# Performance work log

Hardware: AMD Instinct MI355X
Metric: run time of the kernel (lower is better)

Reference implementation:

```python
import jax, jax.numpy as jnp
import numpy as np

B, D, E, C = 16384, 768, 124, 6  # batch, emb_dim, n_experts, n_classes


def _mlp(h, w1, b1, w2, b2):
    # timm Mlp: fc1 -> GELU(exact) -> fc2, hidden = in_features
    return jax.nn.gelu(h @ w1 + b1, approximate=False) @ w2 + b2


def setup_inputs() -> dict:
    key = jax.random.key(0)
    ks = jax.random.split(key, 14)
    s = 0.02
    inp = {
        "x": jax.random.normal(ks[0], (B, D), dtype=jnp.float32),
        # per-sample expert counts in [1, E]
        "n_experts": jax.random.randint(ks[1], (B,), 1, E + 1, dtype=jnp.int64 if jax.config.jax_enable_x64 else jnp.int32),
        # classifier Mlp: D -> D -> E*C
        "cls_w1": jax.random.normal(ks[2], (D, D), dtype=jnp.float32) * s,
        "cls_b1": jnp.zeros((D,), jnp.float32),
        "cls_w2": jax.random.normal(ks[3], (D, E * C), dtype=jnp.float32) * s,
        "cls_b2": jnp.zeros((E * C,), jnp.float32),
        # which_expert Mlp: D -> D -> E
        "we_w1": jax.random.normal(ks[4], (D, D), dtype=jnp.float32) * s,
        "we_b1": jnp.zeros((D,), jnp.float32),
        "we_w2": jax.random.normal(ks[5], (D, E), dtype=jnp.float32) * s,
        "we_b2": jnp.zeros((E,), jnp.float32),
        # expert_weights Mlp: D -> D -> E
        "ew_w1": jax.random.normal(ks[6], (D, D), dtype=jnp.float32) * s,
        "ew_b1": jnp.zeros((D,), jnp.float32),
        "ew_w2": jax.random.normal(ks[7], (D, E), dtype=jnp.float32) * s,
        "ew_b2": jnp.zeros((E,), jnp.float32),
    }
    return inp


def reference(x, n_experts, cls_w1, cls_b1, cls_w2, cls_b2,
              we_w1, we_b1, we_w2, we_b2, ew_w1, ew_b1, ew_w2, ew_b2):
    emb = x  # backbone = identity
    expert_logits = _mlp(emb, cls_w1, cls_b1, cls_w2, cls_b2).reshape(B, E, C)
    expert_weight_logits = _mlp(emb, ew_w1, ew_b1, ew_w2, ew_b2)  # [B, E]
    which_expert = _mlp(emb, we_w1, we_b1, we_w2, we_b2)          # [B, E]

    n = jnp.minimum(n_experts, E)                                  # clamp to n_experts
    # kth_largest: sort descending, pick (n-1)-th per row -> threshold
    sorted_desc = -jnp.sort(-which_expert, axis=1)
    threshold = sorted_desc[jnp.arange(B), n - 1][:, None]         # [B, 1]
    mask = which_expert < threshold

    expert_weight_logits = jnp.where(mask, -jnp.inf, expert_weight_logits)
    expert_proba = jax.nn.softmax(expert_logits, axis=2)           # over classes
    expert_weights = jax.nn.softmax(expert_weight_logits, axis=1)  # over experts

    combined = (expert_proba * expert_weights[:, :, None]).sum(axis=1)
    return combined / expert_weights.sum(axis=1)[:, None]          # [B, C]
```

## Files before the change

kernel.cpp:

```cpp
#include <hip/hip_runtime.h>
#include <stdint.h>

typedef unsigned short u16;
typedef short short8 __attribute__((ext_vector_type(8)));
typedef float f32x4 __attribute__((ext_vector_type(4)));

#define NB 16384

#define OFF_XHI      0ull
#define OFF_XLO      25165824ull
#define OFF_LCLS     0ull
#define OFF_LWE_P0   25165824ull
#define OFF_LWE_P1   33554432ull
#define OFF_BT1      50331648ull
#define OFF_LEWB     50331648ull
#define OFF_BTWE_HI  52690944ull
#define OFF_BTWE_LO  53870592ull
#define OFF_BT2CLS   55050240ull
#define OFF_BT2EW    56229888ull
#define OFF_BT2WE_HI 56426496ull
#define OFF_BT2WE_LO 56623104ull
#define OFF_B1CE     56819712ull
#define OFF_B1WE     56825856ull
#define OFF_B2CLS    56828928ull
#define OFF_B2EW     56832000ull
#define OFF_B2WE     56832512ull
#define OFF_HCLSEW   56833024ull
#define OFF_HWE_HI   107164672ull
#define OFF_HWE_LO   132330496ull
#define WS_NEED      157496320ull

__device__ __forceinline__ u16 f2bf(float f) {
  uint32_t u = __float_as_uint(f);
  u += 0x7fffu + ((u >> 16) & 1u);
  return (u16)(u >> 16);
}
__device__ __forceinline__ float bf2f(u16 h) {
  return __uint_as_float(((uint32_t)h) << 16);
}
__device__ __forceinline__ uint32_t pk2(float a, float b) {
  return (uint32_t)f2bf(a) | ((uint32_t)f2bf(b) << 16);
}
__device__ __forceinline__ void g2l16(const u16* g, u16* l) {
  __builtin_amdgcn_global_load_lds(
      (__attribute__((address_space(1))) void*)(u16*)g,
      (__attribute__((address_space(3))) void*)l, 16, 0, 0);
}

__device__ __forceinline__ float gelu_exact(float v) {
  const float x = fabsf(v) * 0.70710678118654752f;
  const float t = __fdividef(1.0f, __builtin_fmaf(0.3275911f, x, 1.0f));
  float p = __builtin_fmaf(1.061405429f, t, -1.453152027f);
  p = __builtin_fmaf(p, t, 1.421413741f);
  p = __builtin_fmaf(p, t, -0.284496736f);
  p = __builtin_fmaf(p, t, 0.254829592f);
  p = p * t;
  const float e = __expf(-x * x);
  float erfx = __builtin_fmaf(-p, e, 1.0f);
  erfx = (v < 0.f) ? -erfx : erfx;
  return 0.5f * v * (1.0f + erfx);
}

__global__ void prep_all(
    const float* __restrict__ x, u16* __restrict__ xhi, u16* __restrict__ xlo,
    const float* __restrict__ cls_w1, const float* __restrict__ ew_w1,
    const float* __restrict__ we_w1,  const float* __restrict__ cls_w2,
    const float* __restrict__ ew_w2,  const float* __restrict__ we_w2,
    u16* BT1, u16* BTwe_hi, u16* BTwe_lo,
    u16* BT2cls, u16* BT2ew, u16* BT2we_hi, u16* BT2we_lo,
    const float* __restrict__ cls_b1, const float* __restrict__ ew_b1,
    const float* __restrict__ we_b1,  const float* __restrict__ cls_b2,
    const float* __restrict__ ew_b2,  const float* __restrict__ we_b2,
    float* b1ce, float* b1we, float* b2cls, float* b2ew, float* b2we) {
  __shared__ float t[64][65];
  const int bid = blockIdx.x;
  if (bid < 12288) {
    int i = bid * 256 + threadIdx.x;
    float4 v = ((const float4*)x)[i];
    ushort4 h, l;
    h.x = f2bf(v.x); l.x = f2bf(v.x - bf2f(h.x));
    h.y = f2bf(v.y); l.y = f2bf(v.y - bf2f(h.y));
    h.z = f2bf(v.z); l.z = f2bf(v.z - bf2f(h.z));
    h.w = f2bf(v.w); l.w = f2bf(v.w - bf2f(h.w));
    ((ushort4*)xhi)[i] = h;
    ((ushort4*)xlo)[i] = l;
    return;
  }
  if (bid < 13152) {
    const int idx = bid - 12288;
    const int bx = idx % 12, by = (idx / 12) % 12, bz = idx / 144;
    const float* src; int N; u16* dhi; u16* dlo = nullptr;
    switch (bz) {
      case 0: src = cls_w1; N = 768; dhi = BT1; break;
      case 1: src = ew_w1;  N = 768; dhi = BT1 + 768 * 768; break;
      case 2: src = we_w1;  N = 768; dhi = BTwe_hi; dlo = BTwe_lo; break;
      case 3: src = cls_w2; N = 744; dhi = BT2cls; break;
      case 4: src = ew_w2;  N = 124; dhi = BT2ew; break;
      default: src = we_w2; N = 124; dhi = BT2we_hi; dlo = BT2we_lo; break;
    }
    const int Npad = (N + 127) & ~127;
    const int n0 = by * 64;
    if (n0 >= Npad) return;
    const int k0 = bx * 64;
    const int tx = threadIdx.x & 63, tg = threadIdx.x >> 6;
#pragma unroll
    for (int r = 0; r < 16; ++r) {
      int k = tg * 16 + r;
      int n = n0 + tx;
      t[k][tx] = (n < N) ? src[(size_t)(k0 + k) * N + n] : 0.f;
    }
    __syncthreads();
#pragma unroll
    for (int r = 0; r < 16; ++r) {
      int n = n0 + tg * 16 + r;
      if (n < Npad) {
        float v = t[tx][tg * 16 + r];
        u16 h = f2bf(v);
        dhi[(size_t)n * 768 + k0 + tx] = h;
        if (dlo) dlo[(size_t)n * 768 + k0 + tx] = f2bf(v - bf2f(h));
      }
    }
    return;
  }
  int id = (bid - 13152) * 256 + threadIdx.x;
  if (id < 1536) { b1ce[id] = (id < 768) ? cls_b1[id] : ew_b1[id - 768]; return; }
  id -= 1536;
  if (id < 768) { b1we[id] = we_b1[id]; return; }
  id -= 768;
  if (id < 768) { b2cls[id] = (id < 744) ? cls_b2[id] : 0.f; return; }
  id -= 768;
  if (id < 128) { b2ew[id] = (id < 124) ? ew_b2[id] : 0.f; return; }
  id -= 128;
  if (id < 128) { b2we[id] = (id < 124) ? we_b2[id] : 0.f; return; }
}

__device__ __forceinline__ void gemm_core(
    const u16* A0, const u16* A1, const u16* A2, int lda,
    const u16* B0, const u16* B1, const u16* B2,
    int npass, int K, int bm, int tid, u16* sA, u16* sB, f32x4 acc[4][4]) {
  const int lane = tid & 63;
  const int wv = tid >> 6;
  const int wr = wv >> 1, wc = wv & 1;
  const int sr = lane >> 3;
  const int sc = (((lane & 7) ^ sr) << 3);
  for (int p = 0; p < npass; ++p) {
    const u16* A = (p == 0) ? A0 : ((p == 1) ? A1 : A2);
    const u16* Bp = (p == 0) ? B0 : ((p == 1) ? B1 : B2);
    const u16* gA = A + (size_t)(bm + wv * 32 + sr) * lda + sc;
    const u16* gB = Bp + (size_t)(wv * 32 + sr) * K + sc;
    u16* lA = sA + (wv * 32) * 64;
    u16* lB = sB + (wv * 32) * 64;
    for (int kt = 0; kt < K; kt += 64) {
#pragma unroll
      for (int s = 0; s < 4; ++s) {
        g2l16(gA + (size_t)(s * 8) * lda + kt, lA + s * 8 * 64);
        g2l16(gB + (size_t)(s * 8) * K + kt, lB + s * 8 * 64);
      }
      __syncthreads();
#pragma unroll
      for (int ks = 0; ks < 2; ++ks) {
        const int co = ((ks * 4 + (lane >> 4)) ^ (lane & 7)) * 8;
        short8 av[4], bv[4];
#pragma unroll
        for (int i = 0; i < 4; i++)
          av[i] = *(const short8*)(sA + (wr * 64 + i * 16 + (lane & 15)) * 64 + co);
#pragma unroll
        for (int j = 0; j < 4; j++)
          bv[j] = *(const short8*)(sB + (wc * 64 + j * 16 + (lane & 15)) * 64 + co);
#pragma unroll
        for (int i = 0; i < 4; i++)
#pragma unroll
          for (int j = 0; j < 4; j++)
            acc[i][j] = __builtin_amdgcn_mfma_f32_16x16x32_bf16(bv[j], av[i], acc[i][j], 0, 0, 0);
      }
      __syncthreads();
    }
  }
}

__device__ __forceinline__ void gemm_split_core(
    const u16* __restrict__ Ahi, const u16* __restrict__ Alo, int lda,
    const u16* __restrict__ Bhi, const u16* __restrict__ Blo, int ldb,
    int K, int bm, int tid, u16* sA, u16* sB, f32x4 acc[4][4]) {
  const int lane = tid & 63;
  const int wv = tid >> 6;
  const int wr = wv >> 1, wc = wv & 1;
  const int sr = lane >> 3;
  const int gl = (lane & 7) ^ sr;
  const int koff = (gl & 3) << 3;
  const u16* Asel = (gl < 4) ? Ahi : Alo;
  const u16* Bsel = (gl < 4) ? Bhi : Blo;
  const u16* gA = Asel + (size_t)(bm + wv * 32 + sr) * lda + koff;
  const u16* gB = Bsel + (size_t)(wv * 32 + sr) * ldb + koff;
  u16* lA = sA + (wv * 32) * 64;
  u16* lB = sB + (wv * 32) * 64;

  for (int kt = 0; kt < K; kt += 32) {
#pragma unroll
    for (int s = 0; s < 4; ++s) {
      g2l16(gA + (size_t)(s * 8) * lda + kt, lA + s * 8 * 64);
      g2l16(gB + (size_t)(s * 8) * ldb + kt, lB + s * 8 * 64);
    }
    __syncthreads();
    const int coh = (((lane >> 4) ^ (lane & 7)) << 3);
    short8 ah[4], al[4], bh[4], bl[4];
#pragma unroll
    for (int i = 0; i < 4; i++) {
      const u16* p = sA + (wr * 64 + i * 16 + (lane & 15)) * 64;
      ah[i] = *(const short8*)(p + coh);
      al[i] = *(const short8*)(p + (coh ^ 32));
    }
#pragma unroll
    for (int j = 0; j < 4; j++) {
      const u16* p = sB + (wc * 64 + j * 16 + (lane & 15)) * 64;
      bh[j] = *(const short8*)(p + coh);
      bl[j] = *(const short8*)(p + (coh ^ 32));
    }
#pragma unroll
    for (int i = 0; i < 4; i++)
#pragma unroll
      for (int j = 0; j < 4; j++) {
        acc[i][j] = __builtin_amdgcn_mfma_f32_16x16x32_bf16(bh[j], ah[i], acc[i][j], 0, 0, 0);
        acc[i][j] = __builtin_amdgcn_mfma_f32_16x16x32_bf16(bh[j], al[i], acc[i][j], 0, 0, 0);
        acc[i][j] = __builtin_amdgcn_mfma_f32_16x16x32_bf16(bl[j], ah[i], acc[i][j], 0, 0, 0);
      }
    __syncthreads();
  }
}

__device__ __forceinline__ void decode_bid(int bid, int NC, int& bm, int& bn) {
  const int xcd = bid & 7, slot = bid >> 3;
  const int per = NC << 3;
  const int sub = slot / per, rem = slot - sub * per;
  const int colu = rem >> 3, rowIn = rem & 7;
  bm = ((xcd << 4) + (sub << 3) + rowIn) << 7;
  bn = colu << 7;
}

__global__ __launch_bounds__(256, 4) void gemm1_fused(
    const u16* __restrict__ Ahi, const u16* __restrict__ Alo,
    const u16* __restrict__ Bwe_hi, const u16* __restrict__ Bwe_lo,
    const u16* __restrict__ BT1,
    const float* __restrict__ b1we, const float* __restrict__ b1ce,
    u16* __restrict__ out_we_hi, u16* __restrict__ out_we_lo,
    u16* __restrict__ out_ce) {
  __shared__ u16 smem[2 * 128 * 64];
  u16* sA = smem;
  u16* sB = smem + 128 * 64;
  const int tid = threadIdx.x;
  const int lane = tid & 63;
  const int wr = (tid >> 6) >> 1, wc = (tid >> 6) & 1;
  const int K = 768;

  f32x4 acc[4][4];
#pragma unroll
  for (int i = 0; i < 4; i++)
#pragma unroll
    for (int j = 0; j < 4; j++) acc[i][j] = f32x4{0.f, 0.f, 0.f, 0.f};

  if (blockIdx.x < 768) {
    int bm, bn;
    decode_bid(blockIdx.x, 6, bm, bn);
    gemm_split_core(Ahi, Alo, K, Bwe_hi + (size_t)bn * K, Bwe_lo + (size_t)bn * K, K,
                    K, bm, tid, sA, sB, acc);
#pragma unroll
    for (int i = 0; i < 4; i++) {
      const int row = bm + wr * 64 + i * 16 + (lane & 15);
      u16* rh = out_we_hi + (size_t)row * 768;
      u16* rl = out_we_lo + (size_t)row * 768;
#pragma unroll
      for (int j = 0; j < 4; j++) {
        const int colb = bn + wc * 64 + j * 16 + ((lane >> 4) << 2);
        const float4 bs = *(const float4*)(b1we + colb);
        float g0 = gelu_exact(acc[i][j][0] + bs.x);
        float g1 = gelu_exact(acc[i][j][1] + bs.y);
        float g2 = gelu_exact(acc[i][j][2] + bs.z);
        float g3 = gelu_exact(acc[i][j][3] + bs.w);
        uint2 hv, lv;
        u16 h0 = f2bf(g0), h1 = f2bf(g1), h2 = f2bf(g2), h3 = f2bf(g3);
        hv.x = (uint32_t)h0 | ((uint32_t)h1 << 16);
        hv.y = (uint32_t)h2 | ((uint32_t)h3 << 16);
        lv.x = pk2(g0 - bf2f(h0), g1 - bf2f(h1));
        lv.y = pk2(g2 - bf2f(h2), g3 - bf2f(h3));
        *(uint2*)(rh + colb) = hv;
        *(uint2*)(rl + colb) = lv;
      }
    }
  } else {
    int bm, bn;
    decode_bid(blockIdx.x - 768, 12, bm, bn);
    gemm_core(Ahi, nullptr, nullptr, 768, BT1 + (size_t)bn * K, nullptr, nullptr,
              1, K, bm, tid, sA, sB, acc);
#pragma unroll
    for (int i = 0; i < 4; i++) {
      const int row = bm + wr * 64 + i * 16 + (lane & 15);
      u16* ro = out_ce + (size_t)row * 1536;
#pragma unroll
      for (int j = 0; j < 4; j++) {
        const int colb = bn + wc * 64 + j * 16 + ((lane >> 4) << 2);
        const float4 bs = *(const float4*)(b1ce + colb);
        uint2 hv;
        hv.x = pk2(gelu_exact(acc[i][j][0] + bs.x), gelu_exact(acc[i][j][1] + bs.y));
        hv.y = pk2(gelu_exact(acc[i][j][2] + bs.z), gelu_exact(acc[i][j][3] + bs.w));
        *(uint2*)(ro + colb) = hv;
      }
    }
  }
}

__global__ __launch_bounds__(256, 4) void gemm2_fused(
    const u16* __restrict__ h_cls,
    const u16* __restrict__ hwe_hi, const u16* __restrict__ hwe_lo,
    const u16* __restrict__ BT2cls, const u16* __restrict__ BT2ew,
    const u16* __restrict__ BT2we_hi, const u16* __restrict__ BT2we_lo,
    const float* __restrict__ b2cls, const float* __restrict__ b2ew,
    const float* __restrict__ b2we,
    u16* __restrict__ Lcls, u16* __restrict__ LewB,
    float* __restrict__ p0, float* __restrict__ p1) {
  __shared__ u16 sA[128 * 64];
  __shared__ u16 sB[128 * 64];
  const int tid = threadIdx.x;
  const int lane = tid & 63;
  const int wr = (tid >> 6) >> 1, wc = (tid >> 6) & 1;

  f32x4 acc[4][4];
#pragma unroll
  for (int i = 0; i < 4; i++)
#pragma unroll
    for (int j = 0; j < 4; j++) acc[i][j] = f32x4{0.f, 0.f, 0.f, 0.f};

  const int bid = blockIdx.x;
  if (bid < 256) {
    const int half = bid >> 7;
    const int r = bid & 127;
    const int bm = (((r & 7) << 4) + (r >> 3)) << 7;
    const int k0 = half * 384;
    gemm_split_core(hwe_hi + k0, hwe_lo + k0, 768,
                    BT2we_hi + k0, BT2we_lo + k0, 768,
                    384, bm, tid, sA, sB, acc);
    float* o = half ? p1 : p0;
#pragma unroll
    for (int i = 0; i < 4; i++) {
      const int row = bm + wr * 64 + i * 16 + (lane & 15);
#pragma unroll
      for (int j = 0; j < 4; j++) {
        const int colb = wc * 64 + j * 16 + ((lane >> 4) << 2);
        float4 v;
        if (half) {
          v = make_float4(acc[i][j][0], acc[i][j][1], acc[i][j][2], acc[i][j][3]);
        } else {
          const float4 bs = *(const float4*)(b2we + colb);
          v = make_float4(acc[i][j][0] + bs.x, acc[i][j][1] + bs.y,
                          acc[i][j][2] + bs.z, acc[i][j][3] + bs.w);
        }
        *(float4*)(o + (size_t)row * 128 + colb) = v;
      }
    }
  } else if (bid < 1024) {
    int bm, bn;
    decode_bid(bid - 256, 6, bm, bn);
    gemm_core(h_cls, nullptr, nullptr, 1536, BT2cls + (size_t)bn * 768, nullptr, nullptr,
              1, 768, bm, tid, sA, sB, acc);
#pragma unroll
    for (int i = 0; i < 4; i++) {
      const int row = bm + wr * 64 + i * 16 + (lane & 15);
      u16* ro = Lcls + (size_t)row * 768;
#pragma unroll
      for (int j = 0; j < 4; j++) {
        const int colb = bn + wc * 64 + j * 16 + ((lane >> 4) << 2);
        const float4 bs = *(const float4*)(b2cls + colb);
        uint2 hv;
        hv.x = pk2(acc[i][j][0] + bs.x, acc[i][j][1] + bs.y);
        hv.y = pk2(acc[i][j][2] + bs.z, acc[i][j][3] + bs.w);
        *(uint2*)(ro + colb) = hv;
      }
    }
  } else {
    const int r = bid - 1024;
    const int bm = (((r & 7) << 4) + (r >> 3)) << 7;
    gemm_core(h_cls + 768, nullptr, nullptr, 1536, BT2ew, nullptr, nullptr,
              1, 768, bm, tid, sA, sB, acc);
#pragma unroll
    for (int i = 0; i < 4; i++) {
      const int row = bm + wr * 64 + i * 16 + (lane & 15);
      u16* ro = LewB + (size_t)row * 128;
#pragma unroll
      for (int j = 0; j < 4; j++) {
        const int colb = wc * 64 + j * 16 + ((lane >> 4) << 2);
        const float4 bs = *(const float4*)(b2ew + colb);
        uint2 hv;
        hv.x = pk2(acc[i][j][0] + bs.x, acc[i][j][1] + bs.y);
        hv.y = pk2(acc[i][j][2] + bs.z, acc[i][j][3] + bs.w);
        *(uint2*)(ro + colb) = hv;
      }
    }
  }
}

__global__ __launch_bounds__(256) void finalize(
    const u16* __restrict__ Lcls,
    const float* __restrict__ p0, const float* __restrict__ p1,
    const u16* __restrict__ LewB,
    const int* __restrict__ nexp, float* __restrict__ out) {
  const int bid = blockIdx.x;
  const int g = ((bid & 7) << 9) + (bid >> 3);
  const int b = (g << 2) + (int)(threadIdx.x >> 6);
  const int lane = threadIdx.x & 63;
  const float NEG = -3.0e38f;
  const size_t base = (size_t)b * 128;
  const float w0 = (lane < 124) ? (p0[base + lane] + p1[base + lane]) : NEG;
  const float w1 = (lane < 60) ? (p0[base + 64 + lane] + p1[base + 64 + lane]) : NEG;
  int r0 = 0, r1 = 0;
#pragma unroll
  for (int j = 0; j < 64; ++j) {
    float v = __shfl(w0, j, 64);
    r0 += (v > w0); r1 += (v > w1);
  }
#pragma unroll
  for (int j = 0; j < 64; ++j) {
    float v = __shfl(w1, j, 64);
    r0 += (v > w0); r1 += (v > w1);
  }
  int n = nexp[b];
  n = n < 1 ? 1 : (n > 124 ? 124 : n);
  const bool k0 = (lane < 124) && (r0 < n);
  const bool k1 = (lane < 60) && (r1 < n);
  float l0 = k0 ? bf2f(LewB[base + lane]) : NEG;
  float l1 = k1 ? bf2f(LewB[base + 64 + lane]) : NEG;
  float mx = fmaxf(l0, l1);
#pragma unroll
  for (int o = 32; o > 0; o >>= 1) mx = fmaxf(mx, __shfl_xor(mx, o, 64));
  float e0 = k0 ? __expf(l0 - mx) : 0.f;
  float e1 = k1 ? __expf(l1 - mx) : 0.f;
  float S = e0 + e1;
#pragma unroll
  for (int o = 32; o > 0; o >>= 1) S += __shfl_xor(S, o, 64);
  float a0 = 0, a1 = 0, a2 = 0, a3 = 0, a4 = 0, a5 = 0;
#pragma unroll
  for (int h = 0; h < 2; ++h) {
    int e = lane + h * 64;
    float we = h ? e1 : e0;
    if (we > 0.f) {
      const u16* lp = Lcls + (size_t)b * 768 + e * 6;
      float c0 = bf2f(lp[0]), c1 = bf2f(lp[1]), c2 = bf2f(lp[2]);
      float c3 = bf2f(lp[3]), c4 = bf2f(lp[4]), c5 = bf2f(lp[5]);
      float m = fmaxf(fmaxf(fmaxf(c0, c1), fmaxf(c2, c3)), fmaxf(c4, c5));
      float q0 = __expf(c0 - m), q1 = __expf(c1 - m), q2 = __expf(c2 - m);
      float q3 = __expf(c3 - m), q4 = __expf(c4 - m), q5 = __expf(c5 - m);
      float inv = we / (q0 + q1 + q2 + q3 + q4 + q5);
      a0 += q0 * inv; a1 += q1 * inv; a2 += q2 * inv;
      a3 += q3 * inv; a4 += q4 * inv; a5 += q5 * inv;
    }
  }
#pragma unroll
  for (int o = 32; o > 0; o >>= 1) {
    a0 += __shfl_xor(a0, o, 64); a1 += __shfl_xor(a1, o, 64);
    a2 += __shfl_xor(a2, o, 64); a3 += __shfl_xor(a3, o, 64);
    a4 += __shfl_xor(a4, o, 64); a5 += __shfl_xor(a5, o, 64);
  }
  if (lane < 6) {
    float v = (lane == 0) ? a0 : (lane == 1) ? a1 : (lane == 2) ? a2
              : (lane == 3) ? a3 : (lane == 4) ? a4 : a5;
    out[(size_t)b * 6 + lane] = v / S;
  }
}

__global__ void fill_sentinel(float* out, int n, float v) {
  int i = blockIdx.x * 256 + threadIdx.x;
  if (i < n) out[i] = v;
}

extern "C" void kernel_launch(void* const* d_in, const int* in_sizes, int n_in,
                              void* d_out, int out_size, void* d_ws, size_t ws_size,
                              hipStream_t stream) {
  const float* x = (const float*)d_in[0];
  const int* nexp = (const int*)d_in[1];
  const float* cls_w1 = (const float*)d_in[2];
  const float* cls_b1 = (const float*)d_in[3];
  const float* cls_w2 = (const float*)d_in[4];
  const float* cls_b2 = (const float*)d_in[5];
  const float* we_w1 = (const float*)d_in[6];
  const float* we_b1 = (const float*)d_in[7];
  const float* we_w2 = (const float*)d_in[8];
  const float* we_b2 = (const float*)d_in[9];
  const float* ew_w1 = (const float*)d_in[10];
  const float* ew_b1 = (const float*)d_in[11];
  const float* ew_w2 = (const float*)d_in[12];
  const float* ew_b2 = (const float*)d_in[13];
  float* out = (float*)d_out;
  char* ws = (char*)d_ws;

  if (ws_size < WS_NEED) {
    fill_sentinel<<<(out_size + 255) / 256, 256, 0, stream>>>(out, out_size, 12345.0f);
    return;
  }

  u16* xhi = (u16*)(ws + OFF_XHI);
  u16* xlo = (u16*)(ws + OFF_XLO);
  u16* Lcls = (u16*)(ws + OFF_LCLS);
  float* pwe0 = (float*)(ws + OFF_LWE_P0);
  float* pwe1 = (float*)(ws + OFF_LWE_P1);
  u16* LewB = (u16*)(ws + OFF_LEWB);
  u16* BT1 = (u16*)(ws + OFF_BT1);
  u16* BTwe_hi = (u16*)(ws + OFF_BTWE_HI);
  u16* BTwe_lo = (u16*)(ws + OFF_BTWE_LO);
  u16* BT2cls = (u16*)(ws + OFF_BT2CLS);
  u16* BT2ew = (u16*)(ws + OFF_BT2EW);
  u16* BT2we_hi = (u16*)(ws + OFF_BT2WE_HI);
  u16* BT2we_lo = (u16*)(ws + OFF_BT2WE_LO);
  float* b1ce = (float*)(ws + OFF_B1CE);
  float* b1we = (float*)(ws + OFF_B1WE);
  float* b2cls = (float*)(ws + OFF_B2CLS);
  float* b2ew = (float*)(ws + OFF_B2EW);
  float* b2we = (float*)(ws + OFF_B2WE);
  u16* h_clsew = (u16*)(ws + OFF_HCLSEW);
  u16* h_we_hi = (u16*)(ws + OFF_HWE_HI);
  u16* h_we_lo = (u16*)(ws + OFF_HWE_LO);

  prep_all<<<13165, 256, 0, stream>>>(x, xhi, xlo,
                                      cls_w1, ew_w1, we_w1, cls_w2, ew_w2, we_w2,
                                      BT1, BTwe_hi, BTwe_lo, BT2cls, BT2ew, BT2we_hi, BT2we_lo,
                                      cls_b1, ew_b1, we_b1, cls_b2, ew_b2, we_b2,
                                      b1ce, b1we, b2cls, b2ew, b2we);
  gemm1_fused<<<2304, 256, 0, stream>>>(xhi, xlo, BTwe_hi, BTwe_lo, BT1,
                                        b1we, b1ce, h_we_hi, h_we_lo, h_clsew);
  gemm2_fused<<<1152, 256, 0, stream>>>(h_clsew, h_we_hi, h_we_lo,
                                        BT2cls, BT2ew, BT2we_hi, BT2we_lo,
                                        b2cls, b2ew, b2we,
                                        Lcls, LewB, pwe0, pwe1);
  finalize<<<4096, 256, 0, stream>>>(Lcls, pwe0, pwe1, LewB, nexp, out);
}
```

Measured before the change: 337.6 us.

## Fuse which_expert second-layer GEMM into first-layer epilogue with per-tile partial sums

```diff
diff --git a/kernel.cpp b/kernel.cpp
--- a/kernel.cpp
+++ b/kernel.cpp
@@ -10,8 +10,6 @@
 #define OFF_XHI      0ull
 #define OFF_XLO      25165824ull
 #define OFF_LCLS     0ull
-#define OFF_LWE_P0   25165824ull
-#define OFF_LWE_P1   33554432ull
 #define OFF_BT1      50331648ull
 #define OFF_LEWB     50331648ull
 #define OFF_BTWE_HI  52690944ull
@@ -26,9 +24,9 @@
 #define OFF_B2EW     56832000ull
 #define OFF_B2WE     56832512ull
 #define OFF_HCLSEW   56833024ull
-#define OFF_HWE_HI   107164672ull
-#define OFF_HWE_LO   132330496ull
+#define OFF_PWE      107164672ull
 #define WS_NEED      157496320ull
+#define PWE_STRIDE   2097152ull
 
 __device__ __forceinline__ u16 f2bf(float f) {
   uint32_t u = __float_as_uint(f);
@@ -135,46 +133,42 @@
 }
 
 __device__ __forceinline__ void gemm_core(
-    const u16* A0, const u16* A1, const u16* A2, int lda,
-    const u16* B0, const u16* B1, const u16* B2,
-    int npass, int K, int bm, int tid, u16* sA, u16* sB, f32x4 acc[4][4]) {
+    const u16* A0, int lda,
+    const u16* B0,
+    int K, int bm, int tid, u16* sA, u16* sB, f32x4 acc[4][4]) {
   const int lane = tid & 63;
   const int wv = tid >> 6;
   const int wr = wv >> 1, wc = wv & 1;
   const int sr = lane >> 3;
   const int sc = (((lane & 7) ^ sr) << 3);
-  for (int p = 0; p < npass; ++p) {
-    const u16* A = (p == 0) ? A0 : ((p == 1) ? A1 : A2);
-    const u16* Bp = (p == 0) ? B0 : ((p == 1) ? B1 : B2);
-    const u16* gA = A + (size_t)(bm + wv * 32 + sr) * lda + sc;
-    const u16* gB = Bp + (size_t)(wv * 32 + sr) * K + sc;
-    u16* lA = sA + (wv * 32) * 64;
-    u16* lB = sB + (wv * 32) * 64;
-    for (int kt = 0; kt < K; kt += 64) {
-#pragma unroll
-      for (int s = 0; s < 4; ++s) {
-        g2l16(gA + (size_t)(s * 8) * lda + kt, lA + s * 8 * 64);
-        g2l16(gB + (size_t)(s * 8) * K + kt, lB + s * 8 * 64);
-      }
-      __syncthreads();
-#pragma unroll
-      for (int ks = 0; ks < 2; ++ks) {
-        const int co = ((ks * 4 + (lane >> 4)) ^ (lane & 7)) * 8;
-        short8 av[4], bv[4];
-#pragma unroll
-        for (int i = 0; i < 4; i++)
-          av[i] = *(const short8*)(sA + (wr * 64 + i * 16 + (lane & 15)) * 64 + co);
+  const u16* gA = A0 + (size_t)(bm + wv * 32 + sr) * lda + sc;
+  const u16* gB = B0 + (size_t)(wv * 32 + sr) * K + sc;
+  u16* lA = sA + (wv * 32) * 64;
+  u16* lB = sB + (wv * 32) * 64;
+  for (int kt = 0; kt < K; kt += 64) {
+#pragma unroll
+    for (int s = 0; s < 4; ++s) {
+      g2l16(gA + (size_t)(s * 8) * lda + kt, lA + s * 8 * 64);
+      g2l16(gB + (size_t)(s * 8) * K + kt, lB + s * 8 * 64);
+    }
+    __syncthreads();
+#pragma unroll
+    for (int ks = 0; ks < 2; ++ks) {
+      const int co = ((ks * 4 + (lane >> 4)) ^ (lane & 7)) * 8;
+      short8 av[4], bv[4];
+#pragma unroll
+      for (int i = 0; i < 4; i++)
+        av[i] = *(const short8*)(sA + (wr * 64 + i * 16 + (lane & 15)) * 64 + co);
+#pragma unroll
+      for (int j = 0; j < 4; j++)
+        bv[j] = *(const short8*)(sB + (wc * 64 + j * 16 + (lane & 15)) * 64 + co);
+#pragma unroll
+      for (int i = 0; i < 4; i++)
 #pragma unroll
         for (int j = 0; j < 4; j++)
-          bv[j] = *(const short8*)(sB + (wc * 64 + j * 16 + (lane & 15)) * 64 + co);
-#pragma unroll
-        for (int i = 0; i < 4; i++)
-#pragma unroll
-          for (int j = 0; j < 4; j++)
-            acc[i][j] = __builtin_amdgcn_mfma_f32_16x16x32_bf16(bv[j], av[i], acc[i][j], 0, 0, 0);
-      }
-      __syncthreads();
-    }
+          acc[i][j] = __builtin_amdgcn_mfma_f32_16x16x32_bf16(bv[j], av[i], acc[i][j], 0, 0, 0);
+    }
+    __syncthreads();
   }
 }
 
@@ -237,19 +231,22 @@
   bn = colu << 7;
 }
 
-__global__ __launch_bounds__(256, 4) void gemm1_fused(
+__global__ __launch_bounds__(256, 3) void gemm1_fused(
     const u16* __restrict__ Ahi, const u16* __restrict__ Alo,
     const u16* __restrict__ Bwe_hi, const u16* __restrict__ Bwe_lo,
     const u16* __restrict__ BT1,
     const float* __restrict__ b1we, const float* __restrict__ b1ce,
-    u16* __restrict__ out_we_hi, u16* __restrict__ out_we_lo,
+    const u16* __restrict__ BT2we_hi, const u16* __restrict__ BT2we_lo,
+    const float* __restrict__ b2we,
+    float* __restrict__ pwe,
     u16* __restrict__ out_ce) {
   __shared__ u16 smem[2 * 128 * 64];
   u16* sA = smem;
   u16* sB = smem + 128 * 64;
   const int tid = threadIdx.x;
   const int lane = tid & 63;
-  const int wr = (tid >> 6) >> 1, wc = (tid >> 6) & 1;
+  const int wv = tid >> 6;
+  const int wr = wv >> 1, wc = wv & 1;
   const int K = 768;
 
   f32x4 acc[4][4];
@@ -263,41 +260,108 @@
     decode_bid(blockIdx.x, 6, bm, bn);
     gemm_split_core(Ahi, Alo, K, Bwe_hi + (size_t)bn * K, Bwe_lo + (size_t)bn * K, K,
                     K, bm, tid, sA, sB, acc);
+
+    const int lg4 = (lane >> 4) << 2;
+    const int sr = lane >> 3;
+    const int gl = (lane & 7) ^ sr;
+    const int koff = (gl & 3) << 3;
+    const u16* Bsel2 = (gl < 4) ? BT2we_hi : BT2we_lo;
+    const u16* gB2 = Bsel2 + (size_t)(wv * 32 + sr) * 768 + bn + koff;
+    u16* lB = sB + (wv * 32) * 64;
+    const int coh = (((lane >> 4) ^ (lane & 7)) << 3);
+
+    f32x4 acc2[4][4];
+#pragma unroll
+    for (int i = 0; i < 4; i++)
+#pragma unroll
+      for (int j = 0; j < 4; j++) acc2[i][j] = f32x4{0.f, 0.f, 0.f, 0.f};
+
+#pragma unroll
+    for (int c = 0; c < 4; ++c) {
+#pragma unroll
+      for (int s = 0; s < 4; ++s)
+        g2l16(gB2 + (size_t)(s * 8) * 768 + (c << 5), lB + s * 8 * 64);
+      if (wc == (c >> 1)) {
+#pragma unroll
+        for (int i = 0; i < 4; i++) {
+          const int row = wr * 64 + i * 16 + (lane & 15);
+          const int rs = row & 7;
+          u16* lrow = sA + row * 64;
+#pragma unroll
+          for (int jj = 0; jj < 2; jj++) {
+            const int j = ((c & 1) << 1) + jj;
+            const int col = bn + wc * 64 + j * 16 + lg4;
+            const float4 bs = *(const float4*)(b1we + col);
+            float g0 = gelu_exact(acc[i][j][0] + bs.x);
+            float g1 = gelu_exact(acc[i][j][1] + bs.y);
+            float g2 = gelu_exact(acc[i][j][2] + bs.z);
+            float g3 = gelu_exact(acc[i][j][3] + bs.w);
+            u16 h0 = f2bf(g0), h1 = f2bf(g1), h2 = f2bf(g2), h3 = f2bf(g3);
+            uint2 hv, lv;
+            hv.x = (uint32_t)h0 | ((uint32_t)h1 << 16);
+            hv.y = (uint32_t)h2 | ((uint32_t)h3 << 16);
+            lv.x = pk2(g0 - bf2f(h0), g1 - bf2f(h1));
+            lv.y = pk2(g2 - bf2f(h2), g3 - bf2f(h3));
+            const int kk = ((j & 1) << 4) + lg4;
+            const int gr = kk >> 3;
+            const int off = kk & 7;
+            *(uint2*)(lrow + ((gr ^ rs) << 3) + off) = hv;
+            *(uint2*)(lrow + (((gr ^ rs) ^ 4) << 3) + off) = lv;
+          }
+        }
+      }
+      __syncthreads();
+      short8 ah[4], al[4], bh[4], bl[4];
+#pragma unroll
+      for (int i = 0; i < 4; i++) {
+        const u16* p = sA + (wr * 64 + i * 16 + (lane & 15)) * 64;
+        ah[i] = *(const short8*)(p + coh);
+        al[i] = *(const short8*)(p + (coh ^ 32));
+      }
+#pragma unroll
+      for (int j = 0; j < 4; j++) {
+        const u16* p = sB + (wc * 64 + j * 16 + (lane & 15)) * 64;
+        bh[j] = *(const short8*)(p + coh);
+        bl[j] = *(const short8*)(p + (coh ^ 32));
+      }
+#pragma unroll
+      for (int i = 0; i < 4; i++)
+#pragma unroll
+        for (int j = 0; j < 4; j++) {
+          acc2[i][j] = __builtin_amdgcn_mfma_f32_16x16x32_bf16(bh[j], ah[i], acc2[i][j], 0, 0, 0);
+          acc2[i][j] = __builtin_amdgcn_mfma_f32_16x16x32_bf16(bh[j], al[i], acc2[i][j], 0, 0, 0);
+          acc2[i][j] = __builtin_amdgcn_mfma_f32_16x16x32_bf16(bl[j], ah[i], acc2[i][j], 0, 0, 0);
+        }
+      __syncthreads();
+    }
+    const int t = bn >> 7;
+    float* pw = pwe + (size_t)t * PWE_STRIDE;
 #pragma unroll
     for (int i = 0; i < 4; i++) {
       const int row = bm + wr * 64 + i * 16 + (lane & 15);
-      u16* rh = out_we_hi + (size_t)row * 768;
-      u16* rl = out_we_lo + (size_t)row * 768;
 #pragma unroll
       for (int j = 0; j < 4; j++) {
-        const int colb = bn + wc * 64 + j * 16 + ((lane >> 4) << 2);
-        const float4 bs = *(const float4*)(b1we + colb);
-        float g0 = gelu_exact(acc[i][j][0] + bs.x);
-        float g1 = gelu_exact(acc[i][j][1] + bs.y);
-        float g2 = gelu_exact(acc[i][j][2] + bs.z);
-        float g3 = gelu_exact(acc[i][j][3] + bs.w);
-        uint2 hv, lv;
-        u16 h0 = f2bf(g0), h1 = f2bf(g1), h2 = f2bf(g2), h3 = f2bf(g3);
-        hv.x = (uint32_t)h0 | ((uint32_t)h1 << 16);
-        hv.y = (uint32_t)h2 | ((uint32_t)h3 << 16);
-        lv.x = pk2(g0 - bf2f(h0), g1 - bf2f(h1));
-        lv.y = pk2(g2 - bf2f(h2), g3 - bf2f(h3));
-        *(uint2*)(rh + colb) = hv;
-        *(uint2*)(rl + colb) = lv;
+        const int e0 = wc * 64 + j * 16 + lg4;
+        float4 v = make_float4(acc2[i][j][0], acc2[i][j][1], acc2[i][j][2], acc2[i][j][3]);
+        if (t == 0) {
+          const float4 bs = *(const float4*)(b2we + e0);
+          v.x += bs.x; v.y += bs.y; v.z += bs.z; v.w += bs.w;
+        }
+        *(float4*)(pw + (size_t)row * 128 + e0) = v;
       }
     }
   } else {
     int bm, bn;
     decode_bid(blockIdx.x - 768, 12, bm, bn);
-    gemm_core(Ahi, nullptr, nullptr, 768, BT1 + (size_t)bn * K, nullptr, nullptr,
-              1, K, bm, tid, sA, sB, acc);
+    gemm_core(Ahi, 768, BT1 + (size_t)bn * K, K, bm, tid, sA, sB, acc);
+    const int lg4 = (lane >> 4) << 2;
 #pragma unroll
     for (int i = 0; i < 4; i++) {
       const int row = bm + wr * 64 + i * 16 + (lane & 15);
       u16* ro = out_ce + (size_t)row * 1536;
 #pragma unroll
       for (int j = 0; j < 4; j++) {
-        const int colb = bn + wc * 64 + j * 16 + ((lane >> 4) << 2);
+        const int colb = bn + wc * 64 + j * 16 + lg4;
         const float4 bs = *(const float4*)(b1ce + colb);
         uint2 hv;
         hv.x = pk2(gelu_exact(acc[i][j][0] + bs.x), gelu_exact(acc[i][j][1] + bs.y));
@@ -310,18 +374,15 @@
 
 __global__ __launch_bounds__(256, 4) void gemm2_fused(
     const u16* __restrict__ h_cls,
-    const u16* __restrict__ hwe_hi, const u16* __restrict__ hwe_lo,
     const u16* __restrict__ BT2cls, const u16* __restrict__ BT2ew,
-    const u16* __restrict__ BT2we_hi, const u16* __restrict__ BT2we_lo,
     const float* __restrict__ b2cls, const float* __restrict__ b2ew,
-    const float* __restrict__ b2we,
-    u16* __restrict__ Lcls, u16* __restrict__ LewB,
-    float* __restrict__ p0, float* __restrict__ p1) {
+    u16* __restrict__ Lcls, u16* __restrict__ LewB) {
   __shared__ u16 sA[128 * 64];
   __shared__ u16 sB[128 * 64];
   const int tid = threadIdx.x;
   const int lane = tid & 63;
   const int wr = (tid >> 6) >> 1, wc = (tid >> 6) & 1;
+  const int lg4 = (lane >> 4) << 2;
 
   f32x4 acc[4][4];
 #pragma unroll
@@ -330,44 +391,17 @@
     for (int j = 0; j < 4; j++) acc[i][j] = f32x4{0.f, 0.f, 0.f, 0.f};
 
   const int bid = blockIdx.x;
-  if (bid < 256) {
-    const int half = bid >> 7;
-    const int r = bid & 127;
-    const int bm = (((r & 7) << 4) + (r >> 3)) << 7;
-    const int k0 = half * 384;
-    gemm_split_core(hwe_hi + k0, hwe_lo + k0, 768,
-                    BT2we_hi + k0, BT2we_lo + k0, 768,
-                    384, bm, tid, sA, sB, acc);
-    float* o = half ? p1 : p0;
-#pragma unroll
-    for (int i = 0; i < 4; i++) {
-      const int row = bm + wr * 64 + i * 16 + (lane & 15);
-#pragma unroll
-      for (int j = 0; j < 4; j++) {
-        const int colb = wc * 64 + j * 16 + ((lane >> 4) << 2);
-        float4 v;
-        if (half) {
-          v = make_float4(acc[i][j][0], acc[i][j][1], acc[i][j][2], acc[i][j][3]);
-        } else {
-          const float4 bs = *(const float4*)(b2we + colb);
-          v = make_float4(acc[i][j][0] + bs.x, acc[i][j][1] + bs.y,
-                          acc[i][j][2] + bs.z, acc[i][j][3] + bs.w);
-        }
-        *(float4*)(o + (size_t)row * 128 + colb) = v;
-      }
-    }
-  } else if (bid < 1024) {
+  if (bid < 768) {
     int bm, bn;
-    decode_bid(bid - 256, 6, bm, bn);
-    gemm_core(h_cls, nullptr, nullptr, 1536, BT2cls + (size_t)bn * 768, nullptr, nullptr,
-              1, 768, bm, tid, sA, sB, acc);
+    decode_bid(bid, 6, bm, bn);
+    gemm_core(h_cls, 1536, BT2cls + (size_t)bn * 768, 768, bm, tid, sA, sB, acc);
 #pragma unroll
     for (int i = 0; i < 4; i++) {
       const int row = bm + wr * 64 + i * 16 + (lane & 15);
       u16* ro = Lcls + (size_t)row * 768;
 #pragma unroll
       for (int j = 0; j < 4; j++) {
-        const int colb = bn + wc * 64 + j * 16 + ((lane >> 4) << 2);
+        const int colb = bn + wc * 64 + j * 16 + lg4;
         const float4 bs = *(const float4*)(b2cls + colb);
         uint2 hv;
         hv.x = pk2(acc[i][j][0] + bs.x, acc[i][j][1] + bs.y);
@@ -376,17 +410,16 @@
       }
     }
   } else {
-    const int r = bid - 1024;
+    const int r = bid - 768;
     const int bm = (((r & 7) << 4) + (r >> 3)) << 7;
-    gemm_core(h_cls + 768, nullptr, nullptr, 1536, BT2ew, nullptr, nullptr,
-              1, 768, bm, tid, sA, sB, acc);
+    gemm_core(h_cls + 768, 1536, BT2ew, 768, bm, tid, sA, sB, acc);
 #pragma unroll
     for (int i = 0; i < 4; i++) {
       const int row = bm + wr * 64 + i * 16 + (lane & 15);
       u16* ro = LewB + (size_t)row * 128;
 #pragma unroll
       for (int j = 0; j < 4; j++) {
-        const int colb = wc * 64 + j * 16 + ((lane >> 4) << 2);
+        const int colb = wc * 64 + j * 16 + lg4;
         const float4 bs = *(const float4*)(b2ew + colb);
         uint2 hv;
         hv.x = pk2(acc[i][j][0] + bs.x, acc[i][j][1] + bs.y);
@@ -399,7 +432,7 @@
 
 __global__ __launch_bounds__(256) void finalize(
     const u16* __restrict__ Lcls,
-    const float* __restrict__ p0, const float* __restrict__ p1,
+    const float* __restrict__ pwe,
     const u16* __restrict__ LewB,
     const int* __restrict__ nexp, float* __restrict__ out) {
   const int bid = blockIdx.x;
@@ -408,8 +441,17 @@
   const int lane = threadIdx.x & 63;
   const float NEG = -3.0e38f;
   const size_t base = (size_t)b * 128;
-  const float w0 = (lane < 124) ? (p0[base + lane] + p1[base + lane]) : NEG;
-  const float w1 = (lane < 60) ? (p0[base + 64 + lane] + p1[base + 64 + lane]) : NEG;
+  float w0 = NEG, w1 = NEG;
+  if (lane < 124) {
+    const float* q = pwe + base + lane;
+    w0 = q[0] + q[PWE_STRIDE] + q[2 * PWE_STRIDE] + q[3 * PWE_STRIDE]
+       + q[4 * PWE_STRIDE] + q[5 * PWE_STRIDE];
+  }
+  if (lane < 60) {
+    const float* q = pwe + base + 64 + lane;
+    w1 = q[0] + q[PWE_STRIDE] + q[2 * PWE_STRIDE] + q[3 * PWE_STRIDE]
+       + q[4 * PWE_STRIDE] + q[5 * PWE_STRIDE];
+  }
   int r0 = 0, r1 = 0;
 #pragma unroll
   for (int j = 0; j < 64; ++j) {
@@ -498,8 +540,6 @@
   u16* xhi = (u16*)(ws + OFF_XHI);
   u16* xlo = (u16*)(ws + OFF_XLO);
   u16* Lcls = (u16*)(ws + OFF_LCLS);
-  float* pwe0 = (float*)(ws + OFF_LWE_P0);
-  float* pwe1 = (float*)(ws + OFF_LWE_P1);
   u16* LewB = (u16*)(ws + OFF_LEWB);
   u16* BT1 = (u16*)(ws + OFF_BT1);
   u16* BTwe_hi = (u16*)(ws + OFF_BTWE_HI);
@@ -514,8 +554,7 @@
   float* b2ew = (float*)(ws + OFF_B2EW);
   float* b2we = (float*)(ws + OFF_B2WE);
   u16* h_clsew = (u16*)(ws + OFF_HCLSEW);
-  u16* h_we_hi = (u16*)(ws + OFF_HWE_HI);
-  u16* h_we_lo = (u16*)(ws + OFF_HWE_LO);
+  float* pwe = (float*)(ws + OFF_PWE);
 
   prep_all<<<13165, 256, 0, stream>>>(x, xhi, xlo,
                                       cls_w1, ew_w1, we_w1, cls_w2, ew_w2, we_w2,
@@ -523,10 +562,9 @@
                                       cls_b1, ew_b1, we_b1, cls_b2, ew_b2, we_b2,
                                       b1ce, b1we, b2cls, b2ew, b2we);
   gemm1_fused<<<2304, 256, 0, stream>>>(xhi, xlo, BTwe_hi, BTwe_lo, BT1,
-                                        b1we, b1ce, h_we_hi, h_we_lo, h_clsew);
-  gemm2_fused<<<1152, 256, 0, stream>>>(h_clsew, h_we_hi, h_we_lo,
-                                        BT2cls, BT2ew, BT2we_hi, BT2we_lo,
-                                        b2cls, b2ew, b2we,
-                                        Lcls, LewB, pwe0, pwe1);
-  finalize<<<4096, 256, 0, stream>>>(Lcls, pwe0, pwe1, LewB, nexp, out);
-}
+                                        b1we, b1ce, BT2we_hi, BT2we_lo, b2we,
+                                        pwe, h_clsew);
+  gemm2_fused<<<896, 256, 0, stream>>>(h_clsew, BT2cls, BT2ew,
+                                       b2cls, b2ew, Lcls, LewB);
+  finalize<<<4096, 256, 0, stream>>>(Lcls, pwe, LewB, nexp, out);
+}
```

Result: slower. 346.0 us (+2.5%).
